# Kernel tuning notes

Hardware: AMD Instinct MI355X
Metric: run time of the kernel (lower is better)

## Reference

```python
import jax, jax.numpy as jnp
import numpy as np

B, N_H, N_W, DIM, HEADS = 2, 64, 64, 768, 12
HINT = 1024
HIDDEN = DIM * 2       # LTRM expand_ratio = 2
K_ECA = 5              # ECA kernel for C=768: int(|log2(768)/2 + 0.5|)=5 (odd)
TH_LO, TH_HI, MIN_EDGE = 0.02, 0.98, 64


def setup_inputs() -> dict:
    key = jax.random.key(0)
    ks = jax.random.split(key, 12)
    N = N_H * N_W
    x = jax.random.normal(ks[0], (B, N, DIM), jnp.float32)
    # alpha hint: left half = uniform noise (uncertain -> edge tokens),
    # right half = binary blocks aligned to the 16px token cells (easy tokens)
    blocks = (jax.random.uniform(ks[1], (B, 1, N_H, N_W)) > 0.5).astype(jnp.float32)
    blocks_up = jnp.repeat(jnp.repeat(blocks, HINT // N_H, axis=2), HINT // N_W, axis=3)
    noise = jax.random.uniform(ks[2], (B, 1, HINT, HINT))
    col = jnp.arange(HINT)[None, None, None, :]
    alpha_hint = jnp.where(col < HINT // 2, noise, blocks_up)
    s = 0.02
    return {
        "x": x,
        "alpha_hint": alpha_hint,
        # global attention (Hiera-style patched MaskUnitAttention, q_stride=1)
        "qkv_w": jax.random.normal(ks[3], (DIM, 3 * DIM), jnp.float32) * s,
        "qkv_b": jnp.zeros((3 * DIM,), jnp.float32),
        "proj_w": jax.random.normal(ks[4], (DIM, DIM), jnp.float32) * s,
        "proj_b": jnp.zeros((DIM,), jnp.float32),
        # LTRM
        "ln_g": jnp.ones((DIM,), jnp.float32),
        "ln_b": jnp.zeros((DIM,), jnp.float32),
        "fc1_w": jax.random.normal(ks[5], (DIM, HIDDEN), jnp.float32) * s,
        "fc1_b": jnp.zeros((HIDDEN,), jnp.float32),
        "fc2_w": jax.random.normal(ks[6], (HIDDEN, DIM), jnp.float32) * s,  # zeros in ckpt; random for non-trivial math
        "fc2_b": jnp.zeros((DIM,), jnp.float32),
        "eca_w": jax.random.normal(ks[7], (K_ECA,), jnp.float32) * 0.2,
    }


def _edge_mask(alpha_hint):
    # F.interpolate(mode='area') with exact integer factor == block mean
    Bn = alpha_hint.shape[0]
    f_h, f_w = HINT // N_H, HINT // N_W
    hint = alpha_hint.reshape(Bn, N_H, f_h, N_W, f_w).mean(axis=(2, 4)).reshape(Bn, N_H * N_W)
    edge = (hint > TH_LO) & (hint < TH_HI)
    # per-batch fallback: too few edge tokens -> route everything to attention
    edge = jnp.where(edge.sum(axis=1, keepdims=True) < MIN_EDGE, True, edge)
    return edge  # [B, N] bool


def _layernorm(h, g, b, eps=1e-5):
    mu = h.mean(-1, keepdims=True)
    var = ((h - mu) ** 2).mean(-1, keepdims=True)
    return (h - mu) * jax.lax.rsqrt(var + eps) * g + b


def reference(x, alpha_hint, qkv_w, qkv_b, proj_w, proj_b,
              ln_g, ln_b, fc1_w, fc1_b, fc2_w, fc2_b, eca_w):
    Bn, N, C = x.shape
    hd = C // HEADS
    edge = _edge_mask(alpha_hint)                      # [B, N] bool

    # ---- edge path: global SDPA restricted to edge tokens (masked form of
    # the gather->attend->scatter routing: same math, edge keys only) ----
    qkv = (x @ qkv_w + qkv_b).reshape(Bn, N, 3, HEADS, hd)
    q = qkv[:, :, 0].transpose(0, 2, 1, 3)             # [B,H,N,hd]
    k = qkv[:, :, 1].transpose(0, 2, 1, 3)
    v = qkv[:, :, 2].transpose(0, 2, 1, 3)
    scores = jnp.einsum('bhqd,bhkd->bhqk', q, k) / jnp.sqrt(jnp.asarray(hd, x.dtype))
    scores = scores + jnp.where(edge[:, None, None, :], 0.0, -1e9).astype(x.dtype)
    attn = jax.nn.softmax(scores, axis=-1)
    o = jnp.einsum('bhqk,bhkd->bhqd', attn, v)
    o = o.transpose(0, 2, 1, 3).reshape(Bn, N, C)
    attn_out = x + (o @ proj_w + proj_b)               # residual around attention

    # ---- easy path: LTRM (subset of tokens -> DWConv branch skipped,
    # exactly as in LTRM.forward when N != H*W) ----
    h = _layernorm(x, ln_g, ln_b)
    h = jax.nn.gelu(h @ fc1_w + fc1_b, approximate=False)
    h = jax.nn.gelu(h, approximate=False)
    h = h @ fc2_w + fc2_b                              # [B,N,C]
    # ECA: avg-pool over the routed (easy) token set -> masked mean
    easy = ~edge
    cnt = jnp.maximum(easy.sum(axis=1).astype(x.dtype), 1.0)      # [B]
    pooled = (h * easy[..., None]).sum(axis=1) / cnt[:, None]     # [B,C]
    g = jax.lax.conv_general_dilated(
        pooled[:, None, :], eca_w.reshape(1, 1, K_ECA), (1,), 'SAME',
        dimension_numbers=('NCH', 'OIH', 'NCH'))[:, 0, :]          # [B,C]
    h = h * jax.nn.sigmoid(g)[:, None, :]
    ltrm_out = x + h

    # ---- scatter-combine ----
    return jnp.where(edge[..., None], attn_out, ltrm_out)
```

## Files before the change

kernel.cpp:

```cpp
#include <hip/hip_runtime.h>

using u16 = unsigned short;
using short8 = __attribute__((ext_vector_type(8))) short;
using f32x4 = __attribute__((ext_vector_type(4))) float;

#define NTOK 4096
#define CDIM 768
#define QKVD 2304
#define NHEAD 12
#define NSPLIT 4
#define SCALE2 0.18033688011112042f
#define THRRAW 44.3614195558f

__device__ __forceinline__ u16 f2bf(float f) {
  unsigned u = __float_as_uint(f);
  u += 0x7FFFu + ((u >> 16) & 1u);
  return (u16)(u >> 16);
}
__device__ __forceinline__ float bf2f(u16 v) {
  return __uint_as_float(((unsigned)v) << 16);
}
__device__ __forceinline__ float fast_exp2(float x) {
  float r;
  asm("v_exp_f32 %0, %1" : "=v"(r) : "v"(x));
  return r;
}
__device__ __forceinline__ unsigned cvtpk(float lo, float hi) {
  unsigned r;
  asm("v_cvt_pk_bf16_f32 %0, %1, %2" : "=v"(r) : "v"(lo), "v"(hi));
  return r;
}

__device__ __forceinline__ void gload_lds16(const void* g, void* l) {
  __builtin_amdgcn_global_load_lds(
      (__attribute__((address_space(1))) void*)g,
      (__attribute__((address_space(3))) void*)l, 16u, 0, 0u);
}

__device__ __forceinline__ float gelu_exact(float z) {
  return 0.5f * z * (1.0f + erff(z * 0.70710678118654752f));
}

__global__ __launch_bounds__(256) void pool_hint_kernel(
    const float* __restrict__ ah, float* __restrict__ hint)
{
  const int bid = blockIdx.x;
  const int b = bid >> 6, cr = bid & 63;
  const int t = threadIdx.x;
  const float* base = ah + ((size_t)b * 1024 + (size_t)cr * 16) * 1024;
  float s = 0.f;
#pragma unroll
  for (int pr = 0; pr < 16; ++pr) {
    float4 v = *(const float4*)(base + (size_t)pr * 1024 + t * 4);
    s += v.x + v.y + v.z + v.w;
  }
  s += __shfl_xor(s, 1);
  s += __shfl_xor(s, 2);
  if ((t & 3) == 0)
    hint[b * NTOK + cr * 64 + (t >> 2)] = s * (1.f / 256.f);
}

__global__ __launch_bounds__(1024) void finalize_edge_kernel(
    const float* __restrict__ hint, int* __restrict__ edge,
    int* __restrict__ qidx, int* __restrict__ eidx,
    int* __restrict__ cntE, int* __restrict__ cntZ)
{
  const int b = blockIdx.x, t = threadIdx.x;
  __shared__ int wsum[16];
  __shared__ int scntE, scntZ, stot;
  int bits[4]; int s = 0;
#pragma unroll
  for (int j = 0; j < 4; ++j) {
    float h = hint[b * NTOK + t * 4 + j];
    bits[j] = (h > 0.02f && h < 0.98f) ? 1 : 0;
    s += bits[j];
    qidx[b * NTOK + t * 4 + j] = -1;
    eidx[b * NTOK + t * 4 + j] = -1;
  }
  int sw = s;
#pragma unroll
  for (int d = 1; d < 64; d <<= 1) sw += __shfl_xor(sw, d);
  const int l = t & 63, w = t >> 6;
  if (l == 0) wsum[w] = sw;
  if (t == 0) { scntE = 0; scntZ = 0; }
  __syncthreads();
  if (t == 0) { int a = 0; for (int i = 0; i < 16; ++i) a += wsum[i]; stot = a; }
  __syncthreads();
  const bool fb = stot < 64;
#pragma unroll
  for (int j = 0; j < 4; ++j) {
    int e = fb ? 1 : bits[j];
    edge[b * NTOK + t * 4 + j] = e;
    if (e) {
      int p = atomicAdd(&scntE, 1);
      qidx[b * NTOK + p] = t * 4 + j;
    } else {
      int p = atomicAdd(&scntZ, 1);
      eidx[b * NTOK + p] = t * 4 + j;
    }
  }
  __syncthreads();
  if (t == 0) { cntE[b] = scntE; cntZ[b] = scntZ; }
}

__global__ __launch_bounds__(256) void ln_kernel(
    const float* __restrict__ x, const float* __restrict__ gam,
    const float* __restrict__ bet, u16* __restrict__ lnb, u16* __restrict__ xb)
{
  const int row = blockIdx.x, t = threadIdx.x;
  const float* xr = x + (size_t)row * CDIM;
  float v[3];
#pragma unroll
  for (int j = 0; j < 3; ++j) v[j] = xr[t + j * 256];
  float s = v[0] + v[1] + v[2];
  float ss = v[0] * v[0] + v[1] * v[1] + v[2] * v[2];
#pragma unroll
  for (int d = 1; d < 64; d <<= 1) { s += __shfl_xor(s, d); ss += __shfl_xor(ss, d); }
  __shared__ float red[8];
  const int l = t & 63, w = t >> 6;
  if (l == 0) { red[w * 2] = s; red[w * 2 + 1] = ss; }
  __syncthreads();
  s = red[0] + red[2] + red[4] + red[6];
  ss = red[1] + red[3] + red[5] + red[7];
  const float mu = s * (1.f / 768.f);
  const float rstd = rsqrtf(ss * (1.f / 768.f) - mu * mu + 1e-5f);
#pragma unroll
  for (int j = 0; j < 3; ++j) {
    const int cc = t + j * 256;
    lnb[(size_t)row * CDIM + cc] = f2bf((v[j] - mu) * rstd * gam[cc] + bet[cc]);
    xb[(size_t)row * CDIM + cc] = f2bf(v[j]);
  }
}

__global__ __launch_bounds__(256) void transpose_all_kernel(
    const float* __restrict__ qkv_w, const float* __restrict__ proj_w,
    const float* __restrict__ fc1_w, const float* __restrict__ fc2_w,
    u16* __restrict__ qkvT, u16* __restrict__ projT,
    u16* __restrict__ fc1T, u16* __restrict__ fc2T)
{
  __shared__ float tile[32][33];
  int bid = blockIdx.x;
  const float* in; u16* outp; int K, N, bx, by;
  if (bid < 1728)      { in = qkv_w;  outp = qkvT; K = 768;  N = 2304; bx = bid % 72; by = bid / 72; }
  else if (bid < 2304) { bid -= 1728; in = proj_w; outp = projT; K = 768;  N = 768;  bx = bid % 24; by = bid / 24; }
  else if (bid < 3456) { bid -= 2304; in = fc1_w;  outp = fc1T; K = 768;  N = 1536; bx = bid % 48; by = bid / 48; }
  else                 { bid -= 3456; in = fc2_w;  outp = fc2T; K = 1536; N = 768;  bx = bid % 24; by = bid / 24; }
  const int tx = threadIdx.x & 31, ty = threadIdx.x >> 5;
#pragma unroll
  for (int j = 0; j < 32; j += 8)
    tile[ty + j][tx] = in[(size_t)(by * 32 + ty + j) * N + bx * 32 + tx];
  __syncthreads();
#pragma unroll
  for (int j = 0; j < 32; j += 8)
    outp[(size_t)(bx * 32 + ty + j) * K + by * 32 + tx] = f2bf(tile[tx][ty + j]);
}

template <int EPI, bool GATHER_A, bool SCATTER_OUT, int BN>
__global__ __launch_bounds__(256) void gemm_bt(
    const u16* __restrict__ A, const u16* __restrict__ Bt,
    const float* __restrict__ bias, const float* __restrict__ resid,
    const int* __restrict__ list, void* __restrict__ outp, int N, int K)
{
  constexpr int NN = BN / 32;
  const int bm = blockIdx.x, bn = blockIdx.y;
  const int b = bm >> 5, bmi = bm & 31;
  const int rb = bmi * 128;
  if (list[b * NTOK + rb] < 0) return;

  __shared__ __align__(16) u16 lA[128 * 32];
  __shared__ __align__(16) u16 lB[BN * 32];
  const int t = threadIdx.x;
  const int l = t & 63, w = t >> 6;
  const int g = l >> 4, c = l & 15;
  const int wr = w >> 1, wc = w & 1;

  f32x4 acc[4][NN];
#pragma unroll
  for (int i = 0; i < 4; ++i)
#pragma unroll
    for (int j = 0; j < NN; ++j) acc[i][j] = f32x4{0.f, 0.f, 0.f, 0.f};

  const int srow = t >> 2;
  const int sslot = (t & 3) ^ (srow & 3);
  int ta0, ta1;
  if constexpr (GATHER_A) {
    ta0 = list[b * NTOK + rb + srow];       if (ta0 < 0) ta0 = 0;
    ta1 = list[b * NTOK + rb + 64 + srow];  if (ta1 < 0) ta1 = 0;
  } else {
    ta0 = rb + srow;
    ta1 = rb + 64 + srow;
  }
  const u16* gA0 = A + ((size_t)b * NTOK + ta0) * K + sslot * 8;
  const u16* gA1 = A + ((size_t)b * NTOK + ta1) * K + sslot * 8;
  const u16* gB0 = Bt + (size_t)(bn * BN + srow) * K + sslot * 8;
  const u16* gB1 = (BN == 128) ? Bt + (size_t)(bn * BN + 64 + srow) * K + sslot * 8 : nullptr;
  char* ldA = (char*)lA + w * 1024;
  char* ldB = (char*)lB + w * 1024;

  for (int k0 = 0; k0 < K; k0 += 32) {
    __syncthreads();
    gload_lds16(gA0 + k0, ldA);
    gload_lds16(gA1 + k0, ldA + 4096);
    gload_lds16(gB0 + k0, ldB);
    if constexpr (BN == 128) gload_lds16(gB1 + k0, ldB + 4096);
    __syncthreads();
    short8 af[4], bfr[NN];
#pragma unroll
    for (int mi = 0; mi < 4; ++mi) {
      int row = wr * 64 + mi * 16 + c;
      af[mi] = *(const short8*)((const char*)lA + row * 64 + ((g ^ (row & 3)) << 4));
    }
#pragma unroll
    for (int ni = 0; ni < NN; ++ni) {
      int row = wc * (BN / 2) + ni * 16 + c;
      bfr[ni] = *(const short8*)((const char*)lB + row * 64 + ((g ^ (row & 3)) << 4));
    }
#pragma unroll
    for (int mi = 0; mi < 4; ++mi)
#pragma unroll
      for (int ni = 0; ni < NN; ++ni)
        acc[mi][ni] = __builtin_amdgcn_mfma_f32_16x16x32_bf16(af[mi], bfr[ni], acc[mi][ni], 0, 0, 0);
  }

#pragma unroll
  for (int mi = 0; mi < 4; ++mi) {
#pragma unroll
    for (int ni = 0; ni < NN; ++ni) {
      const int col = bn * BN + wc * (BN / 2) + ni * 16 + c;
      const float bv = bias[col];
      const int prow0 = rb + wr * 64 + mi * 16 + g * 4;
#pragma unroll
      for (int r = 0; r < 4; ++r) {
        float v = acc[mi][ni][r] + bv;
        int orow;
        if constexpr (SCATTER_OUT) {
          int tok = list[b * NTOK + prow0 + r];
          if (tok < 0) continue;
          orow = tok;
        } else {
          orow = prow0 + r;
        }
        const size_t idx = ((size_t)b * NTOK + orow) * N + col;
        if constexpr (EPI == 0) {
          ((u16*)outp)[idx] = f2bf(v);
        } else if constexpr (EPI == 1) {
          ((float*)outp)[idx] = v + resid[idx];
        } else if constexpr (EPI == 2) {
          ((u16*)outp)[idx] = f2bf(gelu_exact(gelu_exact(v)));
        } else {
          ((float*)outp)[idx] = v;
        }
      }
    }
  }
}

__global__ __launch_bounds__(64) void flash_part_kernel(
    const u16* __restrict__ qkv, const int* __restrict__ cntE,
    u16* __restrict__ partO, float2* __restrict__ partML)
{
  const int qt = blockIdx.x;
  const int bh = blockIdx.y;
  const int sp = blockIdx.z;
  const int b = bh / NHEAD, h = bh % NHEAD;
  const int cnt = cntE[b];
  if (qt * 32 >= cnt) return;

  const int ntiles = (cnt + 63) >> 6;
  const int per = (ntiles + NSPLIT - 1) / NSPLIT;
  const int tA = sp * per;
  const int tB = min(ntiles, tA + per);
  if (tA >= tB) return;

  __shared__ __align__(16) u16 lV[64 * 64];
  __shared__ __align__(16) u16 lP[32 * 64];

  const int l = threadIdx.x;
  const int g = l >> 4, c = l & 15;
  const int kp = l & 31, dgr = (l >> 5) * 4;
  const size_t tokbase = (size_t)b * NTOK;

  short8 qf[2][2];
#pragma unroll
  for (int mi = 0; mi < 2; ++mi) {
    const int pos = qt * 32 + mi * 16 + c;
    const u16* qp = qkv + (tokbase + pos) * QKVD + h * 64;
#pragma unroll
    for (int kb = 0; kb < 2; ++kb)
      qf[mi][kb] = *(const short8*)(qp + kb * 32 + g * 8);
  }

  f32x4 oacc[2][4];
  float m2run[2], lrun[2];
#pragma unroll
  for (int mi = 0; mi < 2; ++mi) {
#pragma unroll
    for (int nd = 0; nd < 4; ++nd) oacc[mi][nd] = f32x4{0.f, 0.f, 0.f, 0.f};
    m2run[mi] = -1e30f; lrun[mi] = 0.f;
  }

  short8 kS0[4][2], kS1[4][2];

#define LOADK(KS, kt)                                                             \
  {                                                                               \
    const u16* kg = qkv + (tokbase + (kt) * 64 + c) * QKVD + CDIM + h * 64 + g * 8; \
    _Pragma("unroll")                                                             \
    for (int ni = 0; ni < 4; ++ni)                                                \
      _Pragma("unroll")                                                           \
      for (int kb = 0; kb < 2; ++kb)                                              \
        KS[ni][kb] = *(const short8*)(kg + (size_t)(ni * 16) * QKVD + kb * 32);   \
  }

#define FLASH_BODY(KS, kt)                                                        \
  {                                                                               \
    const bool msk = ((kt) * 64 + 64 > cnt);                                      \
    const int rem = cnt - (kt) * 64;                                              \
                   \
    uint4 vv[8];                                                                  \
    {                                                                             \
      const u16* vg = qkv + (tokbase + (kt) * 64 + kp * 2) * QKVD + 2 * CDIM + h * 64 + dgr * 8; \
      _Pragma("unroll")                                                           \
      for (int dbb = 0; dbb < 4; ++dbb) {                                         \
        vv[dbb]     = *(const uint4*)(vg + dbb * 8);                              \
        vv[4 + dbb] = *(const uint4*)(vg + QKVD + dbb * 8);                       \
      }                                                                           \
    }                                                                             \
                                                       \
    f32x4 st[2][4];                                                               \
    __builtin_amdgcn_s_setprio(1);                                                \
    _Pragma("unroll")                                                             \
    for (int mi = 0; mi < 2; ++mi)                                                \
      _Pragma("unroll")                                                           \
      for (int ni = 0; ni < 4; ++ni) {                                            \
        f32x4 sv = f32x4{0.f, 0.f, 0.f, 0.f};                                     \
        sv = __builtin_amdgcn_mfma_f32_16x16x32_bf16(KS[ni][0], qf[mi][0], sv, 0, 0, 0); \
        sv = __builtin_amdgcn_mfma_f32_16x16x32_bf16(KS[ni][1], qf[mi][1], sv, 0, 0, 0); \
        st[mi][ni] = sv;                                                          \
      }                                                                           \
    __builtin_amdgcn_s_setprio(0);                                                \
    if (msk) {                                                                    \
      _Pragma("unroll")                                                           \
      for (int mi = 0; mi < 2; ++mi)                                              \
        _Pragma("unroll")                                                         \
        for (int ni = 0; ni < 4; ++ni)                                            \
          _Pragma("unroll")                                                       \
          for (int r = 0; r < 4; ++r)                                             \
            if (ni * 16 + g * 4 + r >= rem) st[mi][ni][r] = -1e30f;               \
    }                                                                             \
               \
    float mx[2];                                                                  \
    _Pragma("unroll")                                                             \
    for (int mi = 0; mi < 2; ++mi)                                                \
      mx[mi] = fmaxf(                                                             \
          fmaxf(fmaxf(fmaxf(st[mi][0][0], st[mi][0][1]), fmaxf(st[mi][0][2], st[mi][0][3])), \
                fmaxf(fmaxf(st[mi][1][0], st[mi][1][1]), fmaxf(st[mi][1][2], st[mi][1][3]))), \
          fmaxf(fmaxf(fmaxf(st[mi][2][0], st[mi][2][1]), fmaxf(st[mi][2][2], st[mi][2][3])), \
                fmaxf(fmaxf(st[mi][3][0], st[mi][3][1]), fmaxf(st[mi][3][2], st[mi][3][3])))); \
    _Pragma("unroll")                                                             \
    for (int mi = 0; mi < 2; ++mi) mx[mi] = fmaxf(mx[mi], __shfl_xor(mx[mi], 16));\
    _Pragma("unroll")                                                             \
    for (int mi = 0; mi < 2; ++mi) mx[mi] = fmaxf(mx[mi], __shfl_xor(mx[mi], 32));\
    _Pragma("unroll")                                                             \
    for (int mi = 0; mi < 2; ++mi) {                                              \
      if (!__all(mx[mi] - m2run[mi] <= THRRAW)) {                                 \
        const float mnew = fmaxf(m2run[mi], mx[mi]);                              \
        const float alpha = fast_exp2((m2run[mi] - mnew) * SCALE2);               \
        m2run[mi] = mnew;                                                         \
        lrun[mi] *= alpha;                                                        \
        _Pragma("unroll")                                                         \
        for (int nd = 0; nd < 4; ++nd)                                            \
          _Pragma("unroll")                                                       \
          for (int r = 0; r < 4; ++r) oacc[mi][nd][r] *= alpha;                   \
      }                                                                           \
    }                                                                             \
    float rs[2];                                                                  \
    _Pragma("unroll")                                                             \
    for (int mi = 0; mi < 2; ++mi) {                                              \
      const float msc = m2run[mi] * SCALE2;                                       \
      float a = 0.f;                                                              \
      const int qrow = mi * 16 + c;                                               \
      char* pbase = (char*)lP + qrow * 128;                                       \
      const int swz = (qrow & 7) << 4;                                            \
      _Pragma("unroll")                                                           \
      for (int ni = 0; ni < 4; ++ni) {                                            \
        float p0 = fast_exp2(fmaf(st[mi][ni][0], SCALE2, -msc));                  \
        float p1 = fast_exp2(fmaf(st[mi][ni][1], SCALE2, -msc));                  \
        float p2 = fast_exp2(fmaf(st[mi][ni][2], SCALE2, -msc));                  \
        float p3 = fast_exp2(fmaf(st[mi][ni][3], SCALE2, -msc));                  \
        a += (p0 + p1) + (p2 + p3);                                               \
        *(uint2*)(pbase + ((ni * 32 + g * 8) ^ swz)) =                            \
            make_uint2(cvtpk(p0, p1), cvtpk(p2, p3));                             \
      }                                                                           \
      rs[mi] = a;                                                                 \
    }                                                                             \
    _Pragma("unroll")                                                             \
    for (int mi = 0; mi < 2; ++mi) rs[mi] += __shfl_xor(rs[mi], 16);              \
    _Pragma("unroll")                                                             \
    for (int mi = 0; mi < 2; ++mi) rs[mi] += __shfl_xor(rs[mi], 32);              \
    _Pragma("unroll")                                                             \
    for (int mi = 0; mi < 2; ++mi) lrun[mi] += rs[mi];                            \
                 \
    _Pragma("unroll")                                                             \
    for (int dbb = 0; dbb < 4; ++dbb) {                                           \
      union { uint4 q; u16 s[8]; } u0, u1;                                        \
      u0.q = vv[dbb]; u1.q = vv[4 + dbb];                                         \
      const int dd0 = (dgr + dbb) * 8;                                            \
      _Pragma("unroll")                                                           \
      for (int j = 0; j < 8; ++j) {                                               \
        int d = dd0 + j;                                                          \
        *(unsigned*)((char*)lV + d * 128 + ((kp * 4) ^ ((d & 7) << 4))) =         \
            (unsigned)u0.s[j] | ((unsigned)u1.s[j] << 16);                        \
      }                                                                           \
    }                                                                             \
                                                    \
    _Pragma("unroll")                                                             \
    for (int kb = 0; kb < 2; ++kb) {                                              \
      short8 pb[2], vf[4];                                                        \
      _Pragma("unroll")                                                           \
      for (int mi = 0; mi < 2; ++mi) {                                            \
        int qrow = mi * 16 + c;                                                   \
        pb[mi] = *(const short8*)((char*)lP + qrow * 128 +                        \
                                  ((kb * 64 + g * 16) ^ ((qrow & 7) << 4)));      \
      }                                                                           \
      _Pragma("unroll")                                                           \
      for (int nd = 0; nd < 4; ++nd) {                                            \
        int d = nd * 16 + c;                                                      \
        vf[nd] = *(const short8*)((char*)lV + d * 128 +                           \
                                  (((kb * 4 + g) ^ (d & 7)) << 4));               \
      }                                                                           \
      __builtin_amdgcn_s_setprio(1);                                              \
      _Pragma("unroll")                                                           \
      for (int mi = 0; mi < 2; ++mi)                                              \
        _Pragma("unroll")                                                         \
        for (int nd = 0; nd < 4; ++nd)                                            \
          oacc[mi][nd] = __builtin_amdgcn_mfma_f32_16x16x32_bf16(vf[nd], pb[mi], oacc[mi][nd], 0, 0, 0); \
      __builtin_amdgcn_s_setprio(0);                                              \
    }                                                                             \
  }

  LOADK(kS0, tA);
  int kt = tA;
  while (true) {
    if (kt + 1 < tB) LOADK(kS1, kt + 1);
    FLASH_BODY(kS0, kt)
    if (++kt >= tB) break;
    if (kt + 1 < tB) LOADK(kS0, kt + 1);
    FLASH_BODY(kS1, kt)
    if (++kt >= tB) break;
  }
#undef FLASH_BODY
#undef LOADK

  const size_t pobase = ((size_t)(sp * 2 + b) * NHEAD + h) * NTOK;
#pragma unroll
  for (int mi = 0; mi < 2; ++mi) {
    const int pos = qt * 32 + mi * 16 + c;
    if (pos < cnt) {
      u16* op = partO + (pobase + pos) * 64;
#pragma unroll
      for (int nd = 0; nd < 4; ++nd) {
        ushort4 pk4;
        pk4.x = f2bf(oacc[mi][nd][0]);
        pk4.y = f2bf(oacc[mi][nd][1]);
        pk4.z = f2bf(oacc[mi][nd][2]);
        pk4.w = f2bf(oacc[mi][nd][3]);
        *(ushort4*)(op + nd * 16 + g * 4) = pk4;
      }
      if (g == 0)
        partML[pobase + pos] = make_float2(m2run[mi] * SCALE2, lrun[mi]);
    }
  }
}

__global__ __launch_bounds__(256) void flash_merge_kernel(
    const u16* __restrict__ partO, const float2* __restrict__ partML,
    const int* __restrict__ cntE, u16* __restrict__ obf)
{
  const int bh = blockIdx.y;
  const int b = bh / NHEAD, h = bh % NHEAD;
  const int t = threadIdx.x;
  const int pos = blockIdx.x * 4 + (t >> 6);
  const int d = t & 63;
  const int cnt = cntE[b];
  if (pos >= cnt) return;
  const int ntiles = (cnt + 63) >> 6;
  const int per = (ntiles + NSPLIT - 1) / NSPLIT;

  float2 ml[NSPLIT];
  float M = -3e38f;
#pragma unroll
  for (int sp = 0; sp < NSPLIT; ++sp) {
    if (sp * per < ntiles) {
      ml[sp] = partML[((size_t)(sp * 2 + b) * NHEAD + h) * NTOK + pos];
      M = fmaxf(M, ml[sp].x);
    }
  }
  float L = 0.f, O = 0.f;
#pragma unroll
  for (int sp = 0; sp < NSPLIT; ++sp) {
    if (sp * per < ntiles) {
      const float e = fast_exp2(ml[sp].x - M);
      L += ml[sp].y * e;
      O += e * bf2f(partO[(((size_t)(sp * 2 + b) * NHEAD + h) * NTOK + pos) * 64 + d]);
    }
  }
  obf[((size_t)b * NTOK + pos) * CDIM + h * 64 + d] = f2bf(O / L);
}

__global__ __launch_bounds__(256) void pool_partial_kernel(
    const float* __restrict__ h2, const int* __restrict__ edge, float* __restrict__ pooled)
{
  const int bid = blockIdx.x;
  const int b = bid / 48, rm = bid % 48;
  const int cg = rm / 16, ts = rm % 16;
  const int ch = cg * 256 + threadIdx.x;
  float s = 0.f;
  for (int tok = ts * 256; tok < ts * 256 + 256; ++tok) {
    if (!edge[b * NTOK + tok])
      s += h2[((size_t)b * NTOK + tok) * CDIM + ch];
  }
  atomicAdd(&pooled[b * CDIM + ch], s);
}

__global__ void eca_kernel(const float* __restrict__ pooled, const float* __restrict__ w5,
                           const int* __restrict__ ecnt, float* __restrict__ gate)
{
  const int b = blockIdx.x, c = threadIdx.x;
  const float inv = 1.f / fmaxf((float)ecnt[b], 1.f);
  float a = 0.f;
#pragma unroll
  for (int j = 0; j < 5; ++j) {
    int i = c - 2 + j;
    if (i >= 0 && i < CDIM) a += w5[j] * pooled[b * CDIM + i];
  }
  a *= inv;
  gate[b * CDIM + c] = 1.f / (1.f + __expf(-a));
}

__global__ __launch_bounds__(256) void combine_kernel(
    const float* __restrict__ x, const float* __restrict__ attn,
    const float* __restrict__ h2, const float* __restrict__ gate,
    const int* __restrict__ edge, float* __restrict__ out)
{
  const size_t i = ((size_t)blockIdx.x * 256 + threadIdx.x) * 4;
  const int b = (int)(i / ((size_t)NTOK * CDIM));
  const size_t r = i % ((size_t)NTOK * CDIM);
  const int tok = (int)(r / CDIM);
  const int cc = (int)(r % CDIM);
  float4 ov;
  if (edge[b * NTOK + tok]) {
    ov = *(const float4*)(attn + i);
  } else {
    float4 xv = *(const float4*)(x + i);
    float4 hv = *(const float4*)(h2 + i);
    float4 gv = *(const float4*)(gate + b * CDIM + cc);
    ov.x = xv.x + hv.x * gv.x;
    ov.y = xv.y + hv.y * gv.y;
    ov.z = xv.z + hv.z * gv.z;
    ov.w = xv.w + hv.w * gv.w;
  }
  *(float4*)(out + i) = ov;
}

extern "C" void kernel_launch(void* const* d_in, const int* in_sizes, int n_in,
                              void* d_out, int out_size, void* d_ws, size_t ws_size,
                              hipStream_t stream) {
  const float* x      = (const float*)d_in[0];
  const float* ah     = (const float*)d_in[1];
  const float* qkv_w  = (const float*)d_in[2];
  const float* qkv_b  = (const float*)d_in[3];
  const float* proj_w = (const float*)d_in[4];
  const float* proj_b = (const float*)d_in[5];
  const float* ln_g   = (const float*)d_in[6];
  const float* ln_b   = (const float*)d_in[7];
  const float* fc1_w  = (const float*)d_in[8];
  const float* fc1_b  = (const float*)d_in[9];
  const float* fc2_w  = (const float*)d_in[10];
  const float* fc2_b  = (const float*)d_in[11];
  const float* eca_w  = (const float*)d_in[12];
  float* out = (float*)d_out;

  char* ws = (char*)d_ws;
  size_t off = 0;
  auto alloc = [&](size_t bytes) {
    char* p = ws + off;
    off += (bytes + 255) & ~(size_t)255;
    return p;
  };
  float* hint   = (float*)alloc((size_t)2 * NTOK * 4);
  int*   edge   = (int*)alloc((size_t)2 * NTOK * 4);
  int*   qidx   = (int*)alloc((size_t)2 * NTOK * 4);
  int*   eidx   = (int*)alloc((size_t)2 * NTOK * 4);
  int*   cntE   = (int*)alloc(256);
  int*   cntZ   = (int*)alloc(256);
  u16*   xbf    = (u16*)alloc((size_t)2 * NTOK * CDIM * 2);
  u16*   lnbf   = (u16*)alloc((size_t)2 * NTOK * CDIM * 2);
  u16*   qkvT   = (u16*)alloc((size_t)QKVD * CDIM * 2);
  u16*   projT  = (u16*)alloc((size_t)CDIM * CDIM * 2);
  u16*   fc1T   = (u16*)alloc((size_t)1536 * CDIM * 2);
  u16*   fc2T   = (u16*)alloc((size_t)CDIM * 1536 * 2);
  u16*   qkvb   = (u16*)alloc((size_t)2 * NTOK * QKVD * 2);
  u16*   obf    = (u16*)alloc((size_t)2 * NTOK * CDIM * 2);
  u16*   h1bf   = (u16*)alloc((size_t)2 * NTOK * 1536 * 2);
  float* h2     = (float*)alloc((size_t)2 * NTOK * CDIM * 4);
  float* attn   = (float*)alloc((size_t)2 * NTOK * CDIM * 4);
  float* pooled = (float*)alloc((size_t)2 * CDIM * 4);
  float* gate   = (float*)alloc((size_t)2 * CDIM * 4);
  u16*   partO  = (u16*)h1bf;
  float* partML = attn;

  pool_hint_kernel<<<dim3(128), 256, 0, stream>>>(ah, hint);
  finalize_edge_kernel<<<dim3(2), 1024, 0, stream>>>(hint, edge, qidx, eidx, cntE, cntZ);
  ln_kernel<<<dim3(8192), 256, 0, stream>>>(x, ln_g, ln_b, lnbf, xbf);
  transpose_all_kernel<<<dim3(4608), 256, 0, stream>>>(
      qkv_w, proj_w, fc1_w, fc2_w, qkvT, projT, fc1T, fc2T);

  gemm_bt<0, true, false, 128><<<dim3(64, 18), 256, 0, stream>>>(
      xbf, qkvT, qkv_b, nullptr, qidx, qkvb, 2304, 768);
  flash_part_kernel<<<dim3(128, 24, NSPLIT), 64, 0, stream>>>(qkvb, cntE, partO, (float2*)partML);
  flash_merge_kernel<<<dim3(1024, 24), 256, 0, stream>>>(partO, (const float2*)partML, cntE, obf);
  gemm_bt<1, false, true, 64><<<dim3(64, 12), 256, 0, stream>>>(
      obf, projT, proj_b, x, qidx, attn, 768, 768);
  gemm_bt<2, true, false, 128><<<dim3(64, 12), 256, 0, stream>>>(
      lnbf, fc1T, fc1_b, nullptr, eidx, h1bf, 1536, 768);
  gemm_bt<3, false, true, 64><<<dim3(64, 12), 256, 0, stream>>>(
      h1bf, fc2T, fc2_b, nullptr, eidx, h2, 768, 1536);

  hipMemsetAsync(pooled, 0, (size_t)2 * CDIM * 4, stream);
  pool_partial_kernel<<<dim3(96), 256, 0, stream>>>(h2, edge, pooled);
  eca_kernel<<<dim3(2), 768, 0, stream>>>(pooled, eca_w, cntZ, gate);
  combine_kernel<<<dim3(6144), 256, 0, stream>>>(x, attn, h2, gate, edge, out);
}
```

Measured before the change: 461.8 us.

## Write QKV in head-major layout and reorder flash grid to bh-first

The QKV GEMM epilogue now scatters Q, K and V into separate [B*H, N, 64] head-contiguous buffers instead of a token-major [N, 2304] array. The flash kernel reads K/V rows with a 128-byte stride instead of a 4.6KB stride, which improves locality and cache-line use. The grid order is swapped so that blocks sharing a query tile across heads are scheduled adjacently. The cost is a less coalesced GEMM epilogue store, since each 64-column group goes to a different buffer.

New measurement: 458.5 us. No clear change (-0.7%).

```diff
diff --git a/kernel.cpp b/kernel.cpp
--- a/kernel.cpp
+++ b/kernel.cpp
@@ -9,6 +9,7 @@
 #define QKVD 2304
 #define NHEAD 12
 #define NSPLIT 4
+#define QHSZ_ELEM ((size_t)2 * 12 * 4096 * 64)
 #define SCALE2 0.18033688011112042f
 #define THRRAW 44.3614195558f
 
@@ -240,15 +241,23 @@
         } else {
           orow = prow0 + r;
         }
-        const size_t idx = ((size_t)b * NTOK + orow) * N + col;
-        if constexpr (EPI == 0) {
-          ((u16*)outp)[idx] = f2bf(v);
-        } else if constexpr (EPI == 1) {
-          ((float*)outp)[idx] = v + resid[idx];
-        } else if constexpr (EPI == 2) {
-          ((u16*)outp)[idx] = f2bf(gelu_exact(gelu_exact(v)));
+        if constexpr (EPI == 4) {
+          const int h_all = col >> 6;
+          const int sec = (h_all >= 24) ? 2 : (h_all >= 12 ? 1 : 0);
+          const int hh = h_all - sec * 12;
+          ((u16*)outp)[(size_t)sec * QHSZ_ELEM +
+                       (((size_t)(b * 12 + hh) * NTOK + orow) << 6) + (col & 63)] = f2bf(v);
         } else {
-          ((float*)outp)[idx] = v;
+          const size_t idx = ((size_t)b * NTOK + orow) * N + col;
+          if constexpr (EPI == 0) {
+            ((u16*)outp)[idx] = f2bf(v);
+          } else if constexpr (EPI == 1) {
+            ((float*)outp)[idx] = v + resid[idx];
+          } else if constexpr (EPI == 2) {
+            ((u16*)outp)[idx] = f2bf(gelu_exact(gelu_exact(v)));
+          } else if constexpr (EPI == 3) {
+            ((float*)outp)[idx] = v;
+          }
         }
       }
     }
@@ -256,11 +265,11 @@
 }
 
 __global__ __launch_bounds__(64) void flash_part_kernel(
-    const u16* __restrict__ qkv, const int* __restrict__ cntE,
+    const u16* __restrict__ qkvh, const int* __restrict__ cntE,
     u16* __restrict__ partO, float2* __restrict__ partML)
 {
-  const int qt = blockIdx.x;
-  const int bh = blockIdx.y;
+  const int bh = blockIdx.x;
+  const int qt = blockIdx.y;
   const int sp = blockIdx.z;
   const int b = bh / NHEAD, h = bh % NHEAD;
   const int cnt = cntE[b];
@@ -278,13 +287,15 @@
   const int l = threadIdx.x;
   const int g = l >> 4, c = l & 15;
   const int kp = l & 31, dgr = (l >> 5) * 4;
-  const size_t tokbase = (size_t)b * NTOK;
+  const size_t bhbase = (size_t)bh * NTOK * 64;
+  const u16* Qh = qkvh + bhbase;
+  const u16* Kh = qkvh + QHSZ_ELEM + bhbase;
+  const u16* Vh = qkvh + 2 * QHSZ_ELEM + bhbase;
 
   short8 qf[2][2];
 #pragma unroll
   for (int mi = 0; mi < 2; ++mi) {
-    const int pos = qt * 32 + mi * 16 + c;
-    const u16* qp = qkv + (tokbase + pos) * QKVD + h * 64;
+    const u16* qp = Qh + ((size_t)(qt * 32 + mi * 16 + c) << 6);
 #pragma unroll
     for (int kb = 0; kb < 2; ++kb)
       qf[mi][kb] = *(const short8*)(qp + kb * 32 + g * 8);
@@ -303,26 +314,26 @@
 
 #define LOADK(KS, kt)                                                             \
   {                                                                               \
-    const u16* kg = qkv + (tokbase + (kt) * 64 + c) * QKVD + CDIM + h * 64 + g * 8; \
+    const u16* kg = Kh + ((size_t)((kt) * 64 + c) << 6) + g * 8;                  \
     _Pragma("unroll")                                                             \
     for (int ni = 0; ni < 4; ++ni)                                                \
       _Pragma("unroll")                                                           \
       for (int kb = 0; kb < 2; ++kb)                                              \
-        KS[ni][kb] = *(const short8*)(kg + (size_t)(ni * 16) * QKVD + kb * 32);   \
+        KS[ni][kb] = *(const short8*)(kg + ni * 1024 + kb * 32);                  \
   }
 
 #define FLASH_BODY(KS, kt)                                                        \
   {                                                                               \
     const bool msk = ((kt) * 64 + 64 > cnt);                                      \
     const int rem = cnt - (kt) * 64;                                              \
-                   \
+            \
     uint4 vv[8];                                                                  \
     {                                                                             \
-      const u16* vg = qkv + (tokbase + (kt) * 64 + kp * 2) * QKVD + 2 * CDIM + h * 64 + dgr * 8; \
+      const u16* vg = Vh + ((size_t)((kt) * 64 + kp * 2) << 6) + dgr * 8;         \
       _Pragma("unroll")                                                           \
       for (int dbb = 0; dbb < 4; ++dbb) {                                         \
         vv[dbb]     = *(const uint4*)(vg + dbb * 8);                              \
-        vv[4 + dbb] = *(const uint4*)(vg + QKVD + dbb * 8);                       \
+        vv[4 + dbb] = *(const uint4*)(vg + 64 + dbb * 8);                         \
       }                                                                           \
     }                                                                             \
                                                        \
@@ -599,7 +610,7 @@
   u16*   projT  = (u16*)alloc((size_t)CDIM * CDIM * 2);
   u16*   fc1T   = (u16*)alloc((size_t)1536 * CDIM * 2);
   u16*   fc2T   = (u16*)alloc((size_t)CDIM * 1536 * 2);
-  u16*   qkvb   = (u16*)alloc((size_t)2 * NTOK * QKVD * 2);
+  u16*   qkvh   = (u16*)alloc((size_t)3 * QHSZ_ELEM * 2);
   u16*   obf    = (u16*)alloc((size_t)2 * NTOK * CDIM * 2);
   u16*   h1bf   = (u16*)alloc((size_t)2 * NTOK * 1536 * 2);
   float* h2     = (float*)alloc((size_t)2 * NTOK * CDIM * 4);
@@ -615,9 +626,9 @@
   transpose_all_kernel<<<dim3(4608), 256, 0, stream>>>(
       qkv_w, proj_w, fc1_w, fc2_w, qkvT, projT, fc1T, fc2T);
 
-  gemm_bt<0, true, false, 128><<<dim3(64, 18), 256, 0, stream>>>(
-      xbf, qkvT, qkv_b, nullptr, qidx, qkvb, 2304, 768);
-  flash_part_kernel<<<dim3(128, 24, NSPLIT), 64, 0, stream>>>(qkvb, cntE, partO, (float2*)partML);
+  gemm_bt<4, true, false, 128><<<dim3(64, 18), 256, 0, stream>>>(
+      xbf, qkvT, qkv_b, nullptr, qidx, qkvh, 2304, 768);
+  flash_part_kernel<<<dim3(24, 128, NSPLIT), 64, 0, stream>>>(qkvh, cntE, partO, (float2*)partML);
   flash_merge_kernel<<<dim3(1024, 24), 256, 0, stream>>>(partO, (const float2*)partML, cntE, obf);
   gemm_bt<1, false, true, 64><<<dim3(64, 12), 256, 0, stream>>>(
       obf, projT, proj_b, x, qidx, attn, 768, 768);
```
